# Kernel optimization log

Hardware: AMD Instinct MI355X
Metric: run time of the kernel (lower is better)

## Reference

```python
import jax, jax.numpy as jnp
import numpy as np

B, L, E, H = 8192, 64, 128, 8  # batch, max seq len, info_size, head_num
HD = E // H                    # head dim


def setup_inputs() -> dict:
    key = jax.random.key(0)
    k1, k2, k3, k4, k5, k6 = jax.random.split(key, 6)
    inter_info = jax.random.normal(k1, (B, L, E), dtype=jnp.float32)
    # ragged lengths in [1, L] (each sample has at least the query vector)
    lengths = jax.random.randint(k2, (B,), 1, L + 1, dtype=jnp.int32)
    s = 1.0 / np.sqrt(E)
    in_proj_w = jax.random.uniform(k3, (3 * E, E), dtype=jnp.float32, minval=-s, maxval=s)
    in_proj_b = jnp.zeros((3 * E,), dtype=jnp.float32)
    out_proj_w = jax.random.uniform(k4, (E, E), dtype=jnp.float32, minval=-s, maxval=s)
    out_proj_b = jnp.zeros((E,), dtype=jnp.float32)
    return {"inter_info": inter_info, "lengths": lengths,
            "in_proj_w": in_proj_w, "in_proj_b": in_proj_b,
            "out_proj_w": out_proj_w, "out_proj_b": out_proj_b}


def reference(inter_info, lengths, in_proj_w, in_proj_b, out_proj_w, out_proj_b):
    # Per sample: query = first vector, keys/values = all (valid) vectors.
    # Equivalent to torch nn.MultiheadAttention with 1 query per sample.
    Wq, Wk, Wv = in_proj_w[:E], in_proj_w[E:2 * E], in_proj_w[2 * E:]
    bq, bk, bv = in_proj_b[:E], in_proj_b[E:2 * E], in_proj_b[2 * E:]

    query_info = inter_info[:, 0]                                  # [B, E]
    q = (query_info @ Wq.T + bq).reshape(B, H, HD)                 # [B, H, hd]
    k = (inter_info @ Wk.T + bk).reshape(B, L, H, HD)              # [B, L, H, hd]
    v = (inter_info @ Wv.T + bv).reshape(B, L, H, HD)

    scores = jnp.einsum('bhd,blhd->bhl', q, k) / np.sqrt(HD)       # [B, H, L]
    valid = jnp.arange(L)[None, :] < lengths[:, None]              # [B, L]
    scores = jnp.where(valid[:, None, :], scores, -jnp.inf)
    attn = jax.nn.softmax(scores, axis=-1)                         # [B, H, L]

    ctx = jnp.einsum('bhl,blhd->bhd', attn, v).reshape(B, E)       # [B, E]
    attn_hidden = ctx @ out_proj_w.T + out_proj_b                  # [B, E]
    return attn_hidden, query_info
```

## Files before the change

kernel.cpp:

```cpp
#include <hip/hip_runtime.h>
#include <hip/hip_bf16.h>


typedef unsigned int  u32;
typedef unsigned short u16;

#define XR  136
#define XR4 17
#define YR  136
#define UR  136
#define SCR 68

typedef __attribute__((ext_vector_type(8))) __bf16 bf16x8;
typedef __attribute__((ext_vector_type(4))) float  f32x4;

struct __align__(16) Smem {
  u16   Xs[2][64 * XR];
  u16   u[2][8 * UR];
  u16   y[2][8 * YR];
  float q[2][128];
  float sc[2][8][SCR];
  float c[2][8];
  float ctx[2][128];
  int   isbf;
};

__device__ __forceinline__ float blo(u32 u) { return __uint_as_float(u << 16); }
__device__ __forceinline__ float bhi(u32 u) { return __uint_as_float(u & 0xffff0000u); }
__device__ __forceinline__ float b2f(u16 u) { return __uint_as_float(((u32)u) << 16); }
__device__ __forceinline__ u16 f2b(float f) {
  union { __hip_bfloat16 h; u16 u; } cv; cv.h = __float2bfloat16(f); return cv.u;
}
__device__ __forceinline__ u32 pack2(float a, float b) {
  return (u32)f2b(a) | ((u32)f2b(b) << 16);
}
__device__ __forceinline__ void unp8(uint4 v, float* o) {
  o[0]=blo(v.x); o[1]=bhi(v.x); o[2]=blo(v.y); o[3]=bhi(v.y);
  o[4]=blo(v.z); o[5]=bhi(v.z); o[6]=blo(v.w); o[7]=bhi(v.w);
}

template<bool BF>
__device__ __forceinline__ uint4 wfrag(const void* p, size_t off) {
  if (BF) {
    return *(const uint4*)((const u16*)p + off);
  } else {
    const float4* q4 = (const float4*)((const float*)p + off);
    float4 a = q4[0], b = q4[1];
    uint4 v;
    v.x = pack2(a.x, a.y); v.y = pack2(a.z, a.w);
    v.z = pack2(b.x, b.y); v.w = pack2(b.z, b.w);
    return v;
  }
}
template<bool BF>
__device__ __forceinline__ void load4(const void* p, size_t off, float* o) {
  if (BF) {
    uint2 v = *(const uint2*)((const u16*)p + off);
    o[0]=blo(v.x); o[1]=bhi(v.x); o[2]=blo(v.y); o[3]=bhi(v.y);
  } else {
    float4 v = *(const float4*)((const float*)p + off);
    o[0]=v.x; o[1]=v.y; o[2]=v.z; o[3]=v.w;
  }
}
template<bool BF>
__device__ __forceinline__ float lds1(const void* p, size_t off) {
  return BF ? b2f(((const u16*)p)[off]) : ((const float*)p)[off];
}

template<bool BF>
__device__ __forceinline__ void body(Smem& S, int b0, int t,
    const void* inter, const int* lengths, const void* w_in, const void* b_in,
    const void* w_out, const void* b_out, void* out)
{
  const int len0 = lengths[b0];
  const int len1 = lengths[b0 + 1];
  const int lane = t & 63, w = t >> 6;

#pragma unroll
  for (int r = 0; r < 4; ++r) {
    int g = t + 512 * r;
    int tile = g >> 10, gg = g & 1023, l = gg >> 4, ci = gg & 15;
    uint4 v = make_uint4(0u, 0u, 0u, 0u);
    if (l < (tile ? len1 : len0)) {
      if (BF) {
        v = ((const uint4*)inter)[(size_t)b0 * 1024 + g];
      } else {
        const float4* src = (const float4*)inter + (size_t)b0 * 2048;
        float4 a = src[g * 2], b = src[g * 2 + 1];
        v.x = pack2(a.x, a.y); v.y = pack2(a.z, a.w);
        v.z = pack2(b.x, b.y); v.w = pack2(b.z, b.w);
      }
    }
    ((uint4*)S.Xs[tile])[l * XR4 + ci] = v;
  }
  __syncthreads();

  {
    const int e = w * 16 + (lane & 15);
    const int btc = (lane & 15) < 2 ? (lane & 15) : 1;
    const int kb = (lane >> 4) * 8;
    f32x4 acc = {0.f, 0.f, 0.f, 0.f};
#pragma unroll
    for (int kc = 0; kc < 4; ++kc) {
      union { uint4 u4; bf16x8 b; } A, Bf;
      A.u4  = *(const uint4*)&S.Xs[btc][kc * 32 + kb];
      Bf.u4 = wfrag<BF>(w_in, (size_t)e * 128 + kc * 32 + kb);
      acc = __builtin_amdgcn_mfma_f32_16x16x32_bf16(A.b, Bf.b, acc, 0, 0, 0);
    }
    if (lane < 16) {
      float bq = lds1<BF>(b_in, e);
      S.q[0][e] = acc[0] + bq;
      S.q[1][e] = acc[1] + bq;
    }
  }
  __syncthreads();

  {
    const int bt = t >> 8, h = (t >> 5) & 7, cc = t & 31;
    float a0=0.f,a1=0.f,a2=0.f,a3=0.f;
#pragma unroll
    for (int d = 0; d < 16; ++d) {
      float w4[4]; load4<BF>(w_in, (size_t)(128 + h * 16 + d) * 128 + cc * 4, w4);
      float q0 = S.q[bt][h * 16 + d];
      a0 = fmaf(w4[0], q0, a0); a1 = fmaf(w4[1], q0, a1);
      a2 = fmaf(w4[2], q0, a2); a3 = fmaf(w4[3], q0, a3);
    }
    *(uint2*)&S.u[bt][h * UR + cc * 4] = make_uint2(pack2(a0, a1), pack2(a2, a3));
    if (cc == 0) {
      float c0 = 0.f;
      for (int d = 0; d < 16; ++d)
        c0 += S.q[bt][h * 16 + d] * lds1<BF>(b_in, 128 + h * 16 + d);
      S.c[bt][h] = c0;
    }
  }
  __syncthreads();

  {
    const int bt = w >> 2, mt = w & 3;
    const int arow = mt * 16 + (lane & 15);
    const int col  = lane & 15;
    const int kb   = (lane >> 4) * 8;
    const bool hv  = (col < 8);
    f32x4 acc = {0.f, 0.f, 0.f, 0.f};
#pragma unroll
    for (int kc = 0; kc < 4; ++kc) {
      union { uint4 u4; bf16x8 b8; } a, b;
      a.u4 = *(const uint4*)&S.Xs[bt][arow * XR + kc * 32 + kb];
      b.u4 = *(const uint4*)&S.u[bt][(col & 7) * UR + kc * 32 + kb];
      if (!hv) b.u4 = make_uint4(0u, 0u, 0u, 0u);
      acc = __builtin_amdgcn_mfma_f32_16x16x32_bf16(a.b8, b.b8, acc, 0, 0, 0);
    }
    if (hv) {
      const int l0 = mt * 16 + (lane >> 4) * 4;
      const float cadd = S.c[bt][col];
      f32x4 o;
      o[0] = (acc[0] + cadd) * 0.25f;
      o[1] = (acc[1] + cadd) * 0.25f;
      o[2] = (acc[2] + cadd) * 0.25f;
      o[3] = (acc[3] + cadd) * 0.25f;
      *(f32x4*)&S.sc[bt][col][l0] = o;
    }
  }
  __syncthreads();

  {
    const int bt = t >> 8, h = (t >> 5) & 7, sub = t & 31;
    const int len = bt ? len1 : len0;
    const int l0 = sub, l1 = sub + 32;
    float s0 = S.sc[bt][h][l0], s1 = S.sc[bt][h][l1];
    const bool v0 = l0 < len, v1 = l1 < len;
    float m = fmaxf(v0 ? s0 : -INFINITY, v1 ? s1 : -INFINITY);
#pragma unroll
    for (int off = 16; off > 0; off >>= 1) m = fmaxf(m, __shfl_xor(m, off, 32));
    float e0 = v0 ? __expf(s0 - m) : 0.f;
    float e1 = v1 ? __expf(s1 - m) : 0.f;
    float s = e0 + e1;
#pragma unroll
    for (int off = 16; off > 0; off >>= 1) s += __shfl_xor(s, off, 32);
    float inv = 1.f / s;
    S.sc[bt][h][l0] = e0 * inv;
    S.sc[bt][h][l1] = e1 * inv;
  }
  __syncthreads();

  {
    const int bt = w >> 2, j0 = (w & 3) * 32;
    const int hA = (lane & 15) < 8 ? (lane & 15) : 7;
    const int l8 = (lane >> 4) * 8;
    const int jc0 = j0 + (lane & 15), jc1 = jc0 + 16;
    const int len = bt ? len1 : len0;
    f32x4 acc0 = {0.f,0.f,0.f,0.f}, acc1 = {0.f,0.f,0.f,0.f};
    const u16* xb = S.Xs[bt];

    {
      const int lb = l8;
      float4 pa = *(const float4*)&S.sc[bt][hA][lb];
      float4 pb = *(const float4*)&S.sc[bt][hA][lb + 4];
      union { u32 u[4]; bf16x8 b; } A, B0, B1;
      A.u[0] = pack2(pa.x, pa.y); A.u[1] = pack2(pa.z, pa.w);
      A.u[2] = pack2(pb.x, pb.y); A.u[3] = pack2(pb.z, pb.w);
#pragma unroll
      for (int jj = 0; jj < 4; ++jj) {
        u32 lo0 = xb[(lb+2*jj)*XR + jc0], hi0 = xb[(lb+2*jj+1)*XR + jc0];
        u32 lo1 = xb[(lb+2*jj)*XR + jc1], hi1 = xb[(lb+2*jj+1)*XR + jc1];
        B0.u[jj] = lo0 | (hi0 << 16);
        B1.u[jj] = lo1 | (hi1 << 16);
      }
      acc0 = __builtin_amdgcn_mfma_f32_16x16x32_bf16(A.b, B0.b, acc0, 0, 0, 0);
      acc1 = __builtin_amdgcn_mfma_f32_16x16x32_bf16(A.b, B1.b, acc1, 0, 0, 0);
    }
    if (len > 32) {
      const int lb = 32 + l8;
      float4 pa = *(const float4*)&S.sc[bt][hA][lb];
      float4 pb = *(const float4*)&S.sc[bt][hA][lb + 4];
      union { u32 u[4]; bf16x8 b; } A, B0, B1;
      A.u[0] = pack2(pa.x, pa.y); A.u[1] = pack2(pa.z, pa.w);
      A.u[2] = pack2(pb.x, pb.y); A.u[3] = pack2(pb.z, pb.w);
#pragma unroll
      for (int jj = 0; jj < 4; ++jj) {
        u32 lo0 = xb[(lb+2*jj)*XR + jc0], hi0 = xb[(lb+2*jj+1)*XR + jc0];
        u32 lo1 = xb[(lb+2*jj)*XR + jc1], hi1 = xb[(lb+2*jj+1)*XR + jc1];
        B0.u[jj] = lo0 | (hi0 << 16);
        B1.u[jj] = lo1 | (hi1 << 16);
      }
      acc0 = __builtin_amdgcn_mfma_f32_16x16x32_bf16(A.b, B0.b, acc0, 0, 0, 0);
      acc1 = __builtin_amdgcn_mfma_f32_16x16x32_bf16(A.b, B1.b, acc1, 0, 0, 0);
    }
    const int rbase = (lane >> 4) * 4;
    if (rbase < 8) {
#pragma unroll
      for (int r = 0; r < 4; ++r) {
        S.y[bt][(rbase + r) * YR + j0 + (lane & 15)]      = f2b(acc0[r]);
        S.y[bt][(rbase + r) * YR + j0 + 16 + (lane & 15)] = f2b(acc1[r]);
      }
    }
  }
  __syncthreads();

  {
    const int e = w * 16 + (lane & 15);
    const int btc = (lane & 15) < 2 ? (lane & 15) : 1;
    const int kb = (lane >> 4) * 8;
    f32x4 acc = {0.f, 0.f, 0.f, 0.f};
#pragma unroll
    for (int kc = 0; kc < 4; ++kc) {
      union { uint4 u4; bf16x8 b; } A, Bf;
      A.u4  = *(const uint4*)&S.y[btc][w * YR + kc * 32 + kb];
      Bf.u4 = wfrag<BF>(w_in, (size_t)(256 + e) * 128 + kc * 32 + kb);
      acc = __builtin_amdgcn_mfma_f32_16x16x32_bf16(A.b, Bf.b, acc, 0, 0, 0);
    }
    if (lane < 16) {
      float bv = lds1<BF>(b_in, 256 + e);
      S.ctx[0][e] = acc[0] + bv;
      S.ctx[1][e] = acc[1] + bv;
    }
  }
  __syncthreads();

  {
    const int e = w * 16 + (lane & 15);
    const int btc = (lane & 15) < 2 ? (lane & 15) : 1;
    const int kb = (lane >> 4) * 8;
    f32x4 acc = {0.f, 0.f, 0.f, 0.f};
#pragma unroll
    for (int kc = 0; kc < 4; ++kc) {
      union { u32 u[4]; bf16x8 b; } A;
      union { uint4 u4; bf16x8 b; } Bf;
      float4 ca = *(const float4*)&S.ctx[btc][kc * 32 + kb];
      float4 cb = *(const float4*)&S.ctx[btc][kc * 32 + kb + 4];
      A.u[0] = pack2(ca.x, ca.y); A.u[1] = pack2(ca.z, ca.w);
      A.u[2] = pack2(cb.x, cb.y); A.u[3] = pack2(cb.z, cb.w);
      Bf.u4 = wfrag<BF>(w_out, (size_t)e * 128 + kc * 32 + kb);
      acc = __builtin_amdgcn_mfma_f32_16x16x32_bf16(A.b, Bf.b, acc, 0, 0, 0);
    }
    if (lane < 16) {
      float bo = lds1<BF>(b_out, e);
      float a0 = acc[0] + bo, a1 = acc[1] + bo;
      if (BF) {
        ((u16*)out)[(size_t)b0 * 128 + e]       = f2b(a0);
        ((u16*)out)[(size_t)(b0 + 1) * 128 + e] = f2b(a1);
      } else {
        ((float*)out)[(size_t)b0 * 128 + e]       = a0;
        ((float*)out)[(size_t)(b0 + 1) * 128 + e] = a1;
      }
    } else if (lane < 48) {
      const int bt = (lane >> 4) - 1;
      size_t o1 = (size_t)8192 * 128 + (size_t)(b0 + bt) * 128 + e;
      u16 xv = S.Xs[bt][e];
      if (BF) ((u16*)out)[o1] = xv;
      else    ((float*)out)[o1] = b2f(xv);
    }
  }
}

__global__ __launch_bounds__(512, 4) void infoattn_kernel(
    const void* inter, const int* __restrict__ lengths,
    const void* w_in, const void* b_in, const void* w_out, const void* b_out,
    void* out)
{
  __shared__ Smem S;
  const int t = threadIdx.x;
  const int b0 = blockIdx.x * 2;

  if (t < 64) {
    float v = b2f(((const u16*)inter)[t]);
    bool bad = !(fabsf(v) < 1000.f);
    unsigned long long m = __ballot(bad);
    if (t == 0) S.isbf = (m == 0ull) ? 1 : 0;
  }
  __syncthreads();
  const bool isbf = (S.isbf != 0);

  if (isbf) body<true >(S, b0, t, inter, lengths, w_in, b_in, w_out, b_out, out);
  else      body<false>(S, b0, t, inter, lengths, w_in, b_in, w_out, b_out, out);
}

extern "C" void kernel_launch(void* const* d_in, const int* in_sizes, int n_in,
                              void* d_out, int out_size, void* d_ws, size_t ws_size,
                              hipStream_t stream) {
  infoattn_kernel<<<dim3(4096), dim3(512), 0, stream>>>(
      d_in[0], (const int*)d_in[1], d_in[2], d_in[3], d_in[4], d_in[5], d_out);
}
```

Measured before the change: 438.8 us.

## Process one sample per block instead of two, doubling the grid

Each 512-thread block now handles a single batch sample rather than a pair, and the grid grows from 4096 to 8192 blocks. Shared memory per block roughly halves, which could allow more resident blocks per CU. Several stages now run on only half the threads or waves, and the weight fragments are loaded from global memory once per sample instead of being shared across two. The MFMA tiles for the query, value and output projections use one row instead of two, wasting more of each tile.

```diff
diff --git a/kernel.cpp b/kernel.cpp
--- a/kernel.cpp
+++ b/kernel.cpp
@@ -15,13 +15,13 @@
 typedef __attribute__((ext_vector_type(4))) float  f32x4;
 
 struct __align__(16) Smem {
-  u16   Xs[2][64 * XR];
-  u16   u[2][8 * UR];
-  u16   y[2][8 * YR];
-  float q[2][128];
-  float sc[2][8][SCR];
-  float c[2][8];
-  float ctx[2][128];
+  u16   Xs[64 * XR];
+  u16   u[8 * UR];
+  u16   y[8 * YR];
+  float q[128];
+  float sc[8][SCR];
+  float c[8];
+  float ctx[128];
   int   isbf;
 };
 
@@ -33,10 +33,6 @@
 }
 __device__ __forceinline__ u32 pack2(float a, float b) {
   return (u32)f2b(a) | ((u32)f2b(b) << 16);
-}
-__device__ __forceinline__ void unp8(uint4 v, float* o) {
-  o[0]=blo(v.x); o[1]=bhi(v.x); o[2]=blo(v.y); o[3]=bhi(v.y);
-  o[4]=blo(v.z); o[5]=bhi(v.z); o[6]=blo(v.w); o[7]=bhi(v.w);
 }
 
 template<bool BF>
@@ -68,75 +64,69 @@
 }
 
 template<bool BF>
-__device__ __forceinline__ void body(Smem& S, int b0, int t,
+__device__ __forceinline__ void body(Smem& S, int b, int t,
     const void* inter, const int* lengths, const void* w_in, const void* b_in,
     const void* w_out, const void* b_out, void* out)
 {
-  const int len0 = lengths[b0];
-  const int len1 = lengths[b0 + 1];
+  const int len = lengths[b];
   const int lane = t & 63, w = t >> 6;
 
 #pragma unroll
-  for (int r = 0; r < 4; ++r) {
+  for (int r = 0; r < 2; ++r) {
     int g = t + 512 * r;
-    int tile = g >> 10, gg = g & 1023, l = gg >> 4, ci = gg & 15;
+    int l = g >> 4, ci = g & 15;
     uint4 v = make_uint4(0u, 0u, 0u, 0u);
-    if (l < (tile ? len1 : len0)) {
+    if (l < len) {
       if (BF) {
-        v = ((const uint4*)inter)[(size_t)b0 * 1024 + g];
+        v = ((const uint4*)inter)[(size_t)b * 1024 + g];
       } else {
-        const float4* src = (const float4*)inter + (size_t)b0 * 2048;
-        float4 a = src[g * 2], b = src[g * 2 + 1];
+        const float4* src = (const float4*)inter + (size_t)b * 2048;
+        float4 a = src[g * 2], bb = src[g * 2 + 1];
         v.x = pack2(a.x, a.y); v.y = pack2(a.z, a.w);
-        v.z = pack2(b.x, b.y); v.w = pack2(b.z, b.w);
-      }
-    }
-    ((uint4*)S.Xs[tile])[l * XR4 + ci] = v;
+        v.z = pack2(bb.x, bb.y); v.w = pack2(bb.z, bb.w);
+      }
+    }
+    ((uint4*)S.Xs)[l * XR4 + ci] = v;
   }
   __syncthreads();
 
   {
     const int e = w * 16 + (lane & 15);
-    const int btc = (lane & 15) < 2 ? (lane & 15) : 1;
     const int kb = (lane >> 4) * 8;
     f32x4 acc = {0.f, 0.f, 0.f, 0.f};
 #pragma unroll
     for (int kc = 0; kc < 4; ++kc) {
-      union { uint4 u4; bf16x8 b; } A, Bf;
-      A.u4  = *(const uint4*)&S.Xs[btc][kc * 32 + kb];
+      union { uint4 u4; bf16x8 b8; } A, Bf;
+      A.u4  = *(const uint4*)&S.Xs[kc * 32 + kb];
       Bf.u4 = wfrag<BF>(w_in, (size_t)e * 128 + kc * 32 + kb);
-      acc = __builtin_amdgcn_mfma_f32_16x16x32_bf16(A.b, Bf.b, acc, 0, 0, 0);
-    }
-    if (lane < 16) {
-      float bq = lds1<BF>(b_in, e);
-      S.q[0][e] = acc[0] + bq;
-      S.q[1][e] = acc[1] + bq;
-    }
-  }
-  __syncthreads();
-
-  {
-    const int bt = t >> 8, h = (t >> 5) & 7, cc = t & 31;
+      acc = __builtin_amdgcn_mfma_f32_16x16x32_bf16(A.b8, Bf.b8, acc, 0, 0, 0);
+    }
+    if (lane < 16) S.q[e] = acc[0] + lds1<BF>(b_in, e);
+  }
+  __syncthreads();
+
+  if (t < 256) {
+    const int h = t >> 5, cc = t & 31;
     float a0=0.f,a1=0.f,a2=0.f,a3=0.f;
 #pragma unroll
     for (int d = 0; d < 16; ++d) {
       float w4[4]; load4<BF>(w_in, (size_t)(128 + h * 16 + d) * 128 + cc * 4, w4);
-      float q0 = S.q[bt][h * 16 + d];
+      float q0 = S.q[h * 16 + d];
       a0 = fmaf(w4[0], q0, a0); a1 = fmaf(w4[1], q0, a1);
       a2 = fmaf(w4[2], q0, a2); a3 = fmaf(w4[3], q0, a3);
     }
-    *(uint2*)&S.u[bt][h * UR + cc * 4] = make_uint2(pack2(a0, a1), pack2(a2, a3));
+    *(uint2*)&S.u[h * UR + cc * 4] = make_uint2(pack2(a0, a1), pack2(a2, a3));
     if (cc == 0) {
       float c0 = 0.f;
       for (int d = 0; d < 16; ++d)
-        c0 += S.q[bt][h * 16 + d] * lds1<BF>(b_in, 128 + h * 16 + d);
-      S.c[bt][h] = c0;
-    }
-  }
-  __syncthreads();
-
-  {
-    const int bt = w >> 2, mt = w & 3;
+        c0 += S.q[h * 16 + d] * lds1<BF>(b_in, 128 + h * 16 + d);
+      S.c[h] = c0;
+    }
+  }
+  __syncthreads();
+
+  if (w < 4) {
+    const int mt = w;
     const int arow = mt * 16 + (lane & 15);
     const int col  = lane & 15;
     const int kb   = (lane >> 4) * 8;
@@ -144,30 +134,29 @@
     f32x4 acc = {0.f, 0.f, 0.f, 0.f};
 #pragma unroll
     for (int kc = 0; kc < 4; ++kc) {
-      union { uint4 u4; bf16x8 b8; } a, b;
-      a.u4 = *(const uint4*)&S.Xs[bt][arow * XR + kc * 32 + kb];
-      b.u4 = *(const uint4*)&S.u[bt][(col & 7) * UR + kc * 32 + kb];
-      if (!hv) b.u4 = make_uint4(0u, 0u, 0u, 0u);
-      acc = __builtin_amdgcn_mfma_f32_16x16x32_bf16(a.b8, b.b8, acc, 0, 0, 0);
+      union { uint4 u4; bf16x8 b8; } a, bu;
+      a.u4  = *(const uint4*)&S.Xs[arow * XR + kc * 32 + kb];
+      bu.u4 = *(const uint4*)&S.u[(col & 7) * UR + kc * 32 + kb];
+      if (!hv) bu.u4 = make_uint4(0u, 0u, 0u, 0u);
+      acc = __builtin_amdgcn_mfma_f32_16x16x32_bf16(a.b8, bu.b8, acc, 0, 0, 0);
     }
     if (hv) {
       const int l0 = mt * 16 + (lane >> 4) * 4;
-      const float cadd = S.c[bt][col];
+      const float cadd = S.c[col];
       f32x4 o;
       o[0] = (acc[0] + cadd) * 0.25f;
       o[1] = (acc[1] + cadd) * 0.25f;
       o[2] = (acc[2] + cadd) * 0.25f;
       o[3] = (acc[3] + cadd) * 0.25f;
-      *(f32x4*)&S.sc[bt][col][l0] = o;
-    }
-  }
-  __syncthreads();
-
-  {
-    const int bt = t >> 8, h = (t >> 5) & 7, sub = t & 31;
-    const int len = bt ? len1 : len0;
+      *(f32x4*)&S.sc[col][l0] = o;
+    }
+  }
+  __syncthreads();
+
+  if (t < 256) {
+    const int h = t >> 5, sub = t & 31;
     const int l0 = sub, l1 = sub + 32;
-    float s0 = S.sc[bt][h][l0], s1 = S.sc[bt][h][l1];
+    float s0 = S.sc[h][l0], s1 = S.sc[h][l1];
     const bool v0 = l0 < len, v1 = l1 < len;
     float m = fmaxf(v0 ? s0 : -INFINITY, v1 ? s1 : -INFINITY);
 #pragma unroll
@@ -178,24 +167,23 @@
 #pragma unroll
     for (int off = 16; off > 0; off >>= 1) s += __shfl_xor(s, off, 32);
     float inv = 1.f / s;
-    S.sc[bt][h][l0] = e0 * inv;
-    S.sc[bt][h][l1] = e1 * inv;
-  }
-  __syncthreads();
-
-  {
-    const int bt = w >> 2, j0 = (w & 3) * 32;
+    S.sc[h][l0] = e0 * inv;
+    S.sc[h][l1] = e1 * inv;
+  }
+  __syncthreads();
+
+  if (w < 4) {
+    const int j0 = w * 32;
     const int hA = (lane & 15) < 8 ? (lane & 15) : 7;
     const int l8 = (lane >> 4) * 8;
     const int jc0 = j0 + (lane & 15), jc1 = jc0 + 16;
-    const int len = bt ? len1 : len0;
     f32x4 acc0 = {0.f,0.f,0.f,0.f}, acc1 = {0.f,0.f,0.f,0.f};
-    const u16* xb = S.Xs[bt];
+    const u16* xb = S.Xs;
 
     {
       const int lb = l8;
-      float4 pa = *(const float4*)&S.sc[bt][hA][lb];
-      float4 pb = *(const float4*)&S.sc[bt][hA][lb + 4];
+      float4 pa = *(const float4*)&S.sc[hA][lb];
+      float4 pb = *(const float4*)&S.sc[hA][lb + 4];
       union { u32 u[4]; bf16x8 b; } A, B0, B1;
       A.u[0] = pack2(pa.x, pa.y); A.u[1] = pack2(pa.z, pa.w);
       A.u[2] = pack2(pb.x, pb.y); A.u[3] = pack2(pb.z, pb.w);
@@ -211,8 +199,8 @@
     }
     if (len > 32) {
       const int lb = 32 + l8;
-      float4 pa = *(const float4*)&S.sc[bt][hA][lb];
-      float4 pb = *(const float4*)&S.sc[bt][hA][lb + 4];
+      float4 pa = *(const float4*)&S.sc[hA][lb];
+      float4 pb = *(const float4*)&S.sc[hA][lb + 4];
       union { u32 u[4]; bf16x8 b; } A, B0, B1;
       A.u[0] = pack2(pa.x, pa.y); A.u[1] = pack2(pa.z, pa.w);
       A.u[2] = pack2(pb.x, pb.y); A.u[3] = pack2(pb.z, pb.w);
@@ -230,8 +218,8 @@
     if (rbase < 8) {
 #pragma unroll
       for (int r = 0; r < 4; ++r) {
-        S.y[bt][(rbase + r) * YR + j0 + (lane & 15)]      = f2b(acc0[r]);
-        S.y[bt][(rbase + r) * YR + j0 + 16 + (lane & 15)] = f2b(acc1[r]);
+        S.y[(rbase + r) * YR + j0 + (lane & 15)]      = f2b(acc0[r]);
+        S.y[(rbase + r) * YR + j0 + 16 + (lane & 15)] = f2b(acc1[r]);
       }
     }
   }
@@ -239,54 +227,41 @@
 
   {
     const int e = w * 16 + (lane & 15);
-    const int btc = (lane & 15) < 2 ? (lane & 15) : 1;
     const int kb = (lane >> 4) * 8;
     f32x4 acc = {0.f, 0.f, 0.f, 0.f};
 #pragma unroll
     for (int kc = 0; kc < 4; ++kc) {
-      union { uint4 u4; bf16x8 b; } A, Bf;
-      A.u4  = *(const uint4*)&S.y[btc][w * YR + kc * 32 + kb];
+      union { uint4 u4; bf16x8 b8; } A, Bf;
+      A.u4  = *(const uint4*)&S.y[w * YR + kc * 32 + kb];
       Bf.u4 = wfrag<BF>(w_in, (size_t)(256 + e) * 128 + kc * 32 + kb);
-      acc = __builtin_amdgcn_mfma_f32_16x16x32_bf16(A.b, Bf.b, acc, 0, 0, 0);
-    }
-    if (lane < 16) {
-      float bv = lds1<BF>(b_in, 256 + e);
-      S.ctx[0][e] = acc[0] + bv;
-      S.ctx[1][e] = acc[1] + bv;
-    }
+      acc = __builtin_amdgcn_mfma_f32_16x16x32_bf16(A.b8, Bf.b8, acc, 0, 0, 0);
+    }
+    if (lane < 16) S.ctx[e] = acc[0] + lds1<BF>(b_in, 256 + e);
   }
   __syncthreads();
 
   {
     const int e = w * 16 + (lane & 15);
-    const int btc = (lane & 15) < 2 ? (lane & 15) : 1;
     const int kb = (lane >> 4) * 8;
     f32x4 acc = {0.f, 0.f, 0.f, 0.f};
 #pragma unroll
     for (int kc = 0; kc < 4; ++kc) {
       union { u32 u[4]; bf16x8 b; } A;
-      union { uint4 u4; bf16x8 b; } Bf;
-      float4 ca = *(const float4*)&S.ctx[btc][kc * 32 + kb];
-      float4 cb = *(const float4*)&S.ctx[btc][kc * 32 + kb + 4];
+      union { uint4 u4; bf16x8 b8; } Bf;
+      float4 ca = *(const float4*)&S.ctx[kc * 32 + kb];
+      float4 cb = *(const float4*)&S.ctx[kc * 32 + kb + 4];
       A.u[0] = pack2(ca.x, ca.y); A.u[1] = pack2(ca.z, ca.w);
       A.u[2] = pack2(cb.x, cb.y); A.u[3] = pack2(cb.z, cb.w);
       Bf.u4 = wfrag<BF>(w_out, (size_t)e * 128 + kc * 32 + kb);
-      acc = __builtin_amdgcn_mfma_f32_16x16x32_bf16(A.b, Bf.b, acc, 0, 0, 0);
+      acc = __builtin_amdgcn_mfma_f32_16x16x32_bf16(A.b, Bf.b8, acc, 0, 0, 0);
     }
     if (lane < 16) {
-      float bo = lds1<BF>(b_out, e);
-      float a0 = acc[0] + bo, a1 = acc[1] + bo;
-      if (BF) {
-        ((u16*)out)[(size_t)b0 * 128 + e]       = f2b(a0);
-        ((u16*)out)[(size_t)(b0 + 1) * 128 + e] = f2b(a1);
-      } else {
-        ((float*)out)[(size_t)b0 * 128 + e]       = a0;
-        ((float*)out)[(size_t)(b0 + 1) * 128 + e] = a1;
-      }
-    } else if (lane < 48) {
-      const int bt = (lane >> 4) - 1;
-      size_t o1 = (size_t)8192 * 128 + (size_t)(b0 + bt) * 128 + e;
-      u16 xv = S.Xs[bt][e];
+      float a0 = acc[0] + lds1<BF>(b_out, e);
+      if (BF) ((u16*)out)[(size_t)b * 128 + e]   = f2b(a0);
+      else    ((float*)out)[(size_t)b * 128 + e] = a0;
+    } else if (lane < 32) {
+      size_t o1 = (size_t)8192 * 128 + (size_t)b * 128 + e;
+      u16 xv = S.Xs[e];
       if (BF) ((u16*)out)[o1] = xv;
       else    ((float*)out)[o1] = b2f(xv);
     }
@@ -300,7 +275,7 @@
 {
   __shared__ Smem S;
   const int t = threadIdx.x;
-  const int b0 = blockIdx.x * 2;
+  const int b = blockIdx.x;
 
   if (t < 64) {
     float v = b2f(((const u16*)inter)[t]);
@@ -311,13 +286,13 @@
   __syncthreads();
   const bool isbf = (S.isbf != 0);
 
-  if (isbf) body<true >(S, b0, t, inter, lengths, w_in, b_in, w_out, b_out, out);
-  else      body<false>(S, b0, t, inter, lengths, w_in, b_in, w_out, b_out, out);
+  if (isbf) body<true >(S, b, t, inter, lengths, w_in, b_in, w_out, b_out, out);
+  else      body<false>(S, b, t, inter, lengths, w_in, b_in, w_out, b_out, out);
 }
 
 extern "C" void kernel_launch(void* const* d_in, const int* in_sizes, int n_in,
                               void* d_out, int out_size, void* d_ws, size_t ws_size,
                               hipStream_t stream) {
-  infoattn_kernel<<<dim3(4096), dim3(512), 0, stream>>>(
+  infoattn_kernel<<<dim3(8192), dim3(512), 0, stream>>>(
       d_in[0], (const int*)d_in[1], d_in[2], d_in[3], d_in[4], d_in[5], d_out);
 }
```

Result: slower. 530.5 us (+20.9%).

## Split fused attention into three kernels batching projections across more samples

Applied to the files above, without the earlier changes.

Splits the monolithic kernel into three launches. The first computes the q projection and the folded Wk^T q vectors for 8 samples per block. The second does scores, softmax and the P·X product for 2 samples per block, writing the weighted sums to workspace. The third runs the V and output projections for 16 samples per block, so MFMA tiles are fully used and weight loads are shared across more rows. In exchange it adds workspace round-trips through global memory and two extra launches. The old single kernel stays as a fallback when no workspace is provided.

```diff
diff --git a/kernel.cpp b/kernel.cpp
--- a/kernel.cpp
+++ b/kernel.cpp
@@ -4,26 +4,23 @@
 
 typedef unsigned int  u32;
 typedef unsigned short u16;
+typedef unsigned long long u64;
 
 #define XR  136
 #define XR4 17
 #define YR  136
 #define UR  136
 #define SCR 68
+#define QR  132
+#define YSR 1032
+
+#define WS_U_OFF 0u
+#define WS_C_OFF 16777216u
+#define WS_Y_OFF 17825792u
+#define WS_NEED  34603008u
 
 typedef __attribute__((ext_vector_type(8))) __bf16 bf16x8;
 typedef __attribute__((ext_vector_type(4))) float  f32x4;
-
-struct __align__(16) Smem {
-  u16   Xs[2][64 * XR];
-  u16   u[2][8 * UR];
-  u16   y[2][8 * YR];
-  float q[2][128];
-  float sc[2][8][SCR];
-  float c[2][8];
-  float ctx[2][128];
-  int   isbf;
-};
 
 __device__ __forceinline__ float blo(u32 u) { return __uint_as_float(u << 16); }
 __device__ __forceinline__ float bhi(u32 u) { return __uint_as_float(u & 0xffff0000u); }
@@ -33,10 +30,6 @@
 }
 __device__ __forceinline__ u32 pack2(float a, float b) {
   return (u32)f2b(a) | ((u32)f2b(b) << 16);
-}
-__device__ __forceinline__ void unp8(uint4 v, float* o) {
-  o[0]=blo(v.x); o[1]=bhi(v.x); o[2]=blo(v.y); o[3]=bhi(v.y);
-  o[4]=blo(v.z); o[5]=bhi(v.z); o[6]=blo(v.w); o[7]=bhi(v.w);
 }
 
 template<bool BF>
@@ -67,8 +60,375 @@
   return BF ? b2f(((const u16*)p)[off]) : ((const float*)p)[off];
 }
 
+struct __align__(16) SmemK1 {
+  u16   X0s[8 * XR];
+  float q[8 * QR];
+  int   isbf;
+};
+
 template<bool BF>
-__device__ __forceinline__ void body(Smem& S, int b0, int t,
+__device__ __forceinline__ void k1_body(SmemK1& S, int b0, int t,
+    const void* inter, const void* w_in, const void* b_in,
+    u16* Uws, float* Cws)
+{
+  const int lane = t & 63, w = t >> 6;
+
+  if (t < 128) {
+    const int i = t >> 4, ci = t & 15;
+    const size_t bidx = (size_t)(b0 + i);
+    uint4 v;
+    if (BF) {
+      v = ((const uint4*)inter)[bidx * 1024 + ci];
+    } else {
+      const float4* src = (const float4*)inter + bidx * 2048 + ci * 2;
+      float4 a = src[0], b = src[1];
+      v.x = pack2(a.x, a.y); v.y = pack2(a.z, a.w);
+      v.z = pack2(b.x, b.y); v.w = pack2(b.z, b.w);
+    }
+    *(uint4*)&S.X0s[i * XR + ci * 8] = v;
+  }
+  __syncthreads();
+
+  {
+    const int r15 = lane & 15, e = w * 16 + r15;
+    const int kb = (lane >> 4) * 8, rbase = (lane >> 4) * 4;
+    f32x4 acc = {0.f, 0.f, 0.f, 0.f};
+#pragma unroll
+    for (int kc = 0; kc < 4; ++kc) {
+      union { uint4 u4; bf16x8 b8; } A, Bf;
+      A.u4  = *(const uint4*)&S.X0s[(r15 & 7) * XR + kc * 32 + kb];
+      Bf.u4 = wfrag<BF>(w_in, (size_t)e * 128 + kc * 32 + kb);
+      acc = __builtin_amdgcn_mfma_f32_16x16x32_bf16(A.b8, Bf.b8, acc, 0, 0, 0);
+    }
+    const float bq  = lds1<BF>(b_in, e);
+    const float bkv = lds1<BF>(b_in, 128 + e);
+    float cs[4];
+#pragma unroll
+    for (int r = 0; r < 4; ++r) {
+      float qv = acc[r] + bq;
+      if (rbase < 8) S.q[(rbase + r) * QR + e] = qv;
+      cs[r] = qv * bkv;
+    }
+#pragma unroll
+    for (int off = 1; off < 16; off <<= 1) {
+      cs[0] += __shfl_xor(cs[0], off, 64);
+      cs[1] += __shfl_xor(cs[1], off, 64);
+      cs[2] += __shfl_xor(cs[2], off, 64);
+      cs[3] += __shfl_xor(cs[3], off, 64);
+    }
+    if (r15 == 0 && rbase < 8) {
+#pragma unroll
+      for (int r = 0; r < 4; ++r)
+        Cws[(size_t)(b0 + rbase + r) * 8 + w] = cs[r];
+    }
+  }
+  __syncthreads();
+
+  {
+    const int hh = t >> 8, bt = (t >> 5) & 7, cc = t & 31;
+#pragma unroll
+    for (int hi = 0; hi < 4; ++hi) {
+      const int h = hh * 4 + hi;
+      float a0 = 0.f, a1 = 0.f, a2 = 0.f, a3 = 0.f;
+#pragma unroll
+      for (int d = 0; d < 16; ++d) {
+        float w4[4]; load4<BF>(w_in, (size_t)(128 + h * 16 + d) * 128 + cc * 4, w4);
+        float q0 = S.q[bt * QR + h * 16 + d];
+        a0 = fmaf(w4[0], q0, a0); a1 = fmaf(w4[1], q0, a1);
+        a2 = fmaf(w4[2], q0, a2); a3 = fmaf(w4[3], q0, a3);
+      }
+      *(uint2*)&Uws[(size_t)(b0 + bt) * 1024 + h * 128 + cc * 4] =
+          make_uint2(pack2(a0, a1), pack2(a2, a3));
+    }
+  }
+}
+
+__global__ __launch_bounds__(512, 4) void k1_kernel(
+    const void* inter, const void* w_in, const void* b_in,
+    u16* Uws, float* Cws)
+{
+  __shared__ SmemK1 S;
+  const int t = threadIdx.x;
+  const int b0 = blockIdx.x * 8;
+  if (t < 64) {
+    float v = b2f(((const u16*)inter)[t]);
+    bool bad = !(fabsf(v) < 1000.f);
+    u64 m = __ballot(bad);
+    if (t == 0) S.isbf = (m == 0ull) ? 1 : 0;
+  }
+  __syncthreads();
+  if (S.isbf) k1_body<true >(S, b0, t, inter, w_in, b_in, Uws, Cws);
+  else        k1_body<false>(S, b0, t, inter, w_in, b_in, Uws, Cws);
+}
+
+struct __align__(16) SmemK2 {
+  u16   Xs[2][64 * XR];
+  u16   u[2][8 * UR];
+  u16   y[2][8 * YR];
+  float sc[2][8][SCR];
+  float c[2][8];
+  int   isbf;
+};
+
+template<bool BF>
+__device__ __forceinline__ void k2_body(SmemK2& S, int b0, int t,
+    const void* inter, const int* lengths, const u16* Uws, const float* Cws,
+    u16* Yws, void* out)
+{
+  const int len0 = lengths[b0];
+  const int len1 = lengths[b0 + 1];
+  const int lane = t & 63, w = t >> 6;
+
+#pragma unroll
+  for (int r = 0; r < 4; ++r) {
+    int g = t + 512 * r;
+    int tile = g >> 10, gg = g & 1023, l = gg >> 4, ci = gg & 15;
+    uint4 v = make_uint4(0u, 0u, 0u, 0u);
+    if (l < (tile ? len1 : len0)) {
+      if (BF) {
+        v = ((const uint4*)inter)[(size_t)b0 * 1024 + g];
+      } else {
+        const float4* src = (const float4*)inter + (size_t)b0 * 2048;
+        float4 a = src[g * 2], bb = src[g * 2 + 1];
+        v.x = pack2(a.x, a.y); v.y = pack2(a.z, a.w);
+        v.z = pack2(bb.x, bb.y); v.w = pack2(bb.z, bb.w);
+      }
+    }
+    ((uint4*)S.Xs[tile])[l * XR4 + ci] = v;
+  }
+  if (t < 256) {
+    const int bt = t >> 7, rem = t & 127, h = rem >> 4, ci = rem & 15;
+    uint4 v = ((const uint4*)Uws)[(size_t)(b0 + bt) * 128 + h * 16 + ci];
+    *(uint4*)&S.u[bt][h * UR + ci * 8] = v;
+  } else if (t < 272) {
+    const int i = t - 256, bt = i >> 3, h = i & 7;
+    S.c[bt][h] = Cws[(size_t)(b0 + bt) * 8 + h];
+  }
+  __syncthreads();
+
+  {
+    const int bt = w >> 2, mt = w & 3;
+    const int arow = mt * 16 + (lane & 15);
+    const int col  = lane & 15;
+    const int kb   = (lane >> 4) * 8;
+    const bool hv  = (col < 8);
+    f32x4 acc = {0.f, 0.f, 0.f, 0.f};
+#pragma unroll
+    for (int kc = 0; kc < 4; ++kc) {
+      union { uint4 u4; bf16x8 b8; } a, bu;
+      a.u4  = *(const uint4*)&S.Xs[bt][arow * XR + kc * 32 + kb];
+      bu.u4 = *(const uint4*)&S.u[bt][(col & 7) * UR + kc * 32 + kb];
+      if (!hv) bu.u4 = make_uint4(0u, 0u, 0u, 0u);
+      acc = __builtin_amdgcn_mfma_f32_16x16x32_bf16(a.b8, bu.b8, acc, 0, 0, 0);
+    }
+    if (hv) {
+      const int l0 = mt * 16 + (lane >> 4) * 4;
+      const float cadd = S.c[bt][col];
+      f32x4 o;
+      o[0] = (acc[0] + cadd) * 0.25f;
+      o[1] = (acc[1] + cadd) * 0.25f;
+      o[2] = (acc[2] + cadd) * 0.25f;
+      o[3] = (acc[3] + cadd) * 0.25f;
+      *(f32x4*)&S.sc[bt][col][l0] = o;
+    }
+  }
+  __syncthreads();
+
+  {
+    const int bt = t >> 8, h = (t >> 5) & 7, sub = t & 31;
+    const int len = bt ? len1 : len0;
+    const int l0 = sub, l1 = sub + 32;
+    float s0 = S.sc[bt][h][l0], s1 = S.sc[bt][h][l1];
+    const bool v0 = l0 < len, v1 = l1 < len;
+    float m = fmaxf(v0 ? s0 : -INFINITY, v1 ? s1 : -INFINITY);
+#pragma unroll
+    for (int off = 16; off > 0; off >>= 1) m = fmaxf(m, __shfl_xor(m, off, 32));
+    float e0 = v0 ? __expf(s0 - m) : 0.f;
+    float e1 = v1 ? __expf(s1 - m) : 0.f;
+    float s = e0 + e1;
+#pragma unroll
+    for (int off = 16; off > 0; off >>= 1) s += __shfl_xor(s, off, 32);
+    float inv = 1.f / s;
+    S.sc[bt][h][l0] = e0 * inv;
+    S.sc[bt][h][l1] = e1 * inv;
+  }
+  __syncthreads();
+
+  {
+    const int bt = w >> 2, j0 = (w & 3) * 32;
+    const int hA = (lane & 15) < 8 ? (lane & 15) : 7;
+    const int l8 = (lane >> 4) * 8;
+    const int jc0 = j0 + (lane & 15), jc1 = jc0 + 16;
+    const int len = bt ? len1 : len0;
+    f32x4 acc0 = {0.f,0.f,0.f,0.f}, acc1 = {0.f,0.f,0.f,0.f};
+    const u16* xb = S.Xs[bt];
+    {
+      const int lb = l8;
+      float4 pa = *(const float4*)&S.sc[bt][hA][lb];
+      float4 pb = *(const float4*)&S.sc[bt][hA][lb + 4];
+      union { u32 u[4]; bf16x8 b; } A, B0, B1;
+      A.u[0] = pack2(pa.x, pa.y); A.u[1] = pack2(pa.z, pa.w);
+      A.u[2] = pack2(pb.x, pb.y); A.u[3] = pack2(pb.z, pb.w);
+#pragma unroll
+      for (int jj = 0; jj < 4; ++jj) {
+        u32 lo0 = xb[(lb+2*jj)*XR + jc0], hi0 = xb[(lb+2*jj+1)*XR + jc0];
+        u32 lo1 = xb[(lb+2*jj)*XR + jc1], hi1 = xb[(lb+2*jj+1)*XR + jc1];
+        B0.u[jj] = lo0 | (hi0 << 16);
+        B1.u[jj] = lo1 | (hi1 << 16);
+      }
+      acc0 = __builtin_amdgcn_mfma_f32_16x16x32_bf16(A.b, B0.b, acc0, 0, 0, 0);
+      acc1 = __builtin_amdgcn_mfma_f32_16x16x32_bf16(A.b, B1.b, acc1, 0, 0, 0);
+    }
+    if (len > 32) {
+      const int lb = 32 + l8;
+      float4 pa = *(const float4*)&S.sc[bt][hA][lb];
+      float4 pb = *(const float4*)&S.sc[bt][hA][lb + 4];
+      union { u32 u[4]; bf16x8 b; } A, B0, B1;
+      A.u[0] = pack2(pa.x, pa.y); A.u[1] = pack2(pa.z, pa.w);
+      A.u[2] = pack2(pb.x, pb.y); A.u[3] = pack2(pb.z, pb.w);
+#pragma unroll
+      for (int jj = 0; jj < 4; ++jj) {
+        u32 lo0 = xb[(lb+2*jj)*XR + jc0], hi0 = xb[(lb+2*jj+1)*XR + jc0];
+        u32 lo1 = xb[(lb+2*jj)*XR + jc1], hi1 = xb[(lb+2*jj+1)*XR + jc1];
+        B0.u[jj] = lo0 | (hi0 << 16);
+        B1.u[jj] = lo1 | (hi1 << 16);
+      }
+      acc0 = __builtin_amdgcn_mfma_f32_16x16x32_bf16(A.b, B0.b, acc0, 0, 0, 0);
+      acc1 = __builtin_amdgcn_mfma_f32_16x16x32_bf16(A.b, B1.b, acc1, 0, 0, 0);
+    }
+    const int rbase = (lane >> 4) * 4;
+    if (rbase < 8) {
+#pragma unroll
+      for (int r = 0; r < 4; ++r) {
+        S.y[bt][(rbase + r) * YR + j0 + (lane & 15)]      = f2b(acc0[r]);
+        S.y[bt][(rbase + r) * YR + j0 + 16 + (lane & 15)] = f2b(acc1[r]);
+      }
+    }
+  }
+  __syncthreads();
+
+  if (t < 256) {
+    const int bt = t >> 7, rem = t & 127, h = rem >> 4, ci = rem & 15;
+    uint4 v = *(const uint4*)&S.y[bt][h * YR + ci * 8];
+    ((uint4*)Yws)[(size_t)(b0 + bt) * 128 + h * 16 + ci] = v;
+  } else {
+    const int i = t - 256, bt = i >> 7, e = i & 127;
+    size_t o1 = (size_t)8192 * 128 + (size_t)(b0 + bt) * 128 + e;
+    u16 xv = S.Xs[bt][e];
+    if (BF) ((u16*)out)[o1] = xv;
+    else    ((float*)out)[o1] = b2f(xv);
+  }
+}
+
+__global__ __launch_bounds__(512, 4) void k2_kernel(
+    const void* inter, const int* __restrict__ lengths,
+    const u16* Uws, const float* Cws, u16* Yws, void* out)
+{
+  __shared__ SmemK2 S;
+  const int t = threadIdx.x;
+  const int b0 = blockIdx.x * 2;
+  if (t < 64) {
+    float v = b2f(((const u16*)inter)[t]);
+    bool bad = !(fabsf(v) < 1000.f);
+    u64 m = __ballot(bad);
+    if (t == 0) S.isbf = (m == 0ull) ? 1 : 0;
+  }
+  __syncthreads();
+  if (S.isbf) k2_body<true >(S, b0, t, inter, lengths, Uws, Cws, Yws, out);
+  else        k2_body<false>(S, b0, t, inter, lengths, Uws, Cws, Yws, out);
+}
+
+struct __align__(16) SmemK3 {
+  u16 ys[16 * YSR];
+  u16 ctx[16 * 136];
+  int isbf;
+};
+
+template<bool BF>
+__device__ __forceinline__ void k3_body(SmemK3& S, int b0, int t,
+    const u16* Yws, const void* w_in, const void* b_in,
+    const void* w_out, const void* b_out, void* out)
+{
+  const int lane = t & 63, w = t >> 6;
+
+#pragma unroll
+  for (int r = 0; r < 4; ++r) {
+    int idx = t + 512 * r;
+    int row = idx >> 7, ci = idx & 127;
+    uint4 v = ((const uint4*)Yws)[(size_t)(b0 + row) * 128 + ci];
+    *(uint4*)&S.ys[row * YSR + ci * 8] = v;
+  }
+  __syncthreads();
+
+  {
+    const int col = lane & 15, kb = (lane >> 4) * 8, rbase = (lane >> 4) * 4;
+    f32x4 acc = {0.f, 0.f, 0.f, 0.f};
+#pragma unroll
+    for (int kc = 0; kc < 4; ++kc) {
+      union { uint4 u4; bf16x8 b8; } A, Bf;
+      A.u4  = *(const uint4*)&S.ys[col * YSR + w * 128 + kc * 32 + kb];
+      Bf.u4 = wfrag<BF>(w_in, (size_t)(256 + w * 16 + col) * 128 + kc * 32 + kb);
+      acc = __builtin_amdgcn_mfma_f32_16x16x32_bf16(A.b8, Bf.b8, acc, 0, 0, 0);
+    }
+    const float bv = lds1<BF>(b_in, 256 + w * 16 + col);
+#pragma unroll
+    for (int r = 0; r < 4; ++r)
+      S.ctx[(rbase + r) * 136 + w * 16 + col] = f2b(acc[r] + bv);
+  }
+  __syncthreads();
+
+  {
+    const int col = lane & 15, kb = (lane >> 4) * 8, rbase = (lane >> 4) * 4;
+    f32x4 acc = {0.f, 0.f, 0.f, 0.f};
+#pragma unroll
+    for (int kc = 0; kc < 4; ++kc) {
+      union { uint4 u4; bf16x8 b8; } A, Bf;
+      A.u4  = *(const uint4*)&S.ctx[col * 136 + kc * 32 + kb];
+      Bf.u4 = wfrag<BF>(w_out, (size_t)(w * 16 + col) * 128 + kc * 32 + kb);
+      acc = __builtin_amdgcn_mfma_f32_16x16x32_bf16(A.b8, Bf.b8, acc, 0, 0, 0);
+    }
+    const float bo = lds1<BF>(b_out, w * 16 + col);
+#pragma unroll
+    for (int r = 0; r < 4; ++r) {
+      float v = acc[r] + bo;
+      size_t oo = (size_t)(b0 + rbase + r) * 128 + w * 16 + col;
+      if (BF) ((u16*)out)[oo] = f2b(v);
+      else    ((float*)out)[oo] = v;
+    }
+  }
+}
+
+__global__ __launch_bounds__(512, 4) void k3_kernel(
+    const u16* Yws, const void* w_in, const void* b_in,
+    const void* w_out, const void* b_out, void* out)
+{
+  __shared__ SmemK3 S;
+  const int t = threadIdx.x;
+  const int b0 = blockIdx.x * 16;
+  if (t < 64) {
+    float v = b2f(((const u16*)w_out)[t]);
+    bool bad = !(fabsf(v) < 1000.f);
+    u64 m = __ballot(bad);
+    if (t == 0) S.isbf = (m == 0ull) ? 1 : 0;
+  }
+  __syncthreads();
+  if (S.isbf) k3_body<true >(S, b0, t, Yws, w_in, b_in, w_out, b_out, out);
+  else        k3_body<false>(S, b0, t, Yws, w_in, b_in, w_out, b_out, out);
+}
+
+struct __align__(16) SmemM {
+  u16   Xs[2][64 * XR];
+  u16   u[2][8 * UR];
+  u16   y[2][8 * YR];
+  float q[2][128];
+  float sc[2][8][SCR];
+  float c[2][8];
+  float ctx[2][128];
+  int   isbf;
+};
+
+template<bool BF>
+__device__ __forceinline__ void mono_body(SmemM& S, int b0, int t,
     const void* inter, const int* lengths, const void* w_in, const void* b_in,
     const void* w_out, const void* b_out, void* out)
 {
@@ -102,10 +462,10 @@
     f32x4 acc = {0.f, 0.f, 0.f, 0.f};
 #pragma unroll
     for (int kc = 0; kc < 4; ++kc) {
-      union { uint4 u4; bf16x8 b; } A, Bf;
+      union { uint4 u4; bf16x8 b8; } A, Bf;
       A.u4  = *(const uint4*)&S.Xs[btc][kc * 32 + kb];
       Bf.u4 = wfrag<BF>(w_in, (size_t)e * 128 + kc * 32 + kb);
-      acc = __builtin_amdgcn_mfma_f32_16x16x32_bf16(A.b, Bf.b, acc, 0, 0, 0);
+      acc = __builtin_amdgcn_mfma_f32_16x16x32_bf16(A.b8, Bf.b8, acc, 0, 0, 0);
     }
     if (lane < 16) {
       float bq = lds1<BF>(b_in, e);
@@ -144,11 +504,11 @@
     f32x4 acc = {0.f, 0.f, 0.f, 0.f};
 #pragma unroll
     for (int kc = 0; kc < 4; ++kc) {
-      union { uint4 u4; bf16x8 b8; } a, b;
-      a.u4 = *(const uint4*)&S.Xs[bt][arow * XR + kc * 32 + kb];
-      b.u4 = *(const uint4*)&S.u[bt][(col & 7) * UR + kc * 32 + kb];
-      if (!hv) b.u4 = make_uint4(0u, 0u, 0u, 0u);
-      acc = __builtin_amdgcn_mfma_f32_16x16x32_bf16(a.b8, b.b8, acc, 0, 0, 0);
+      union { uint4 u4; bf16x8 b8; } a, bu;
+      a.u4  = *(const uint4*)&S.Xs[bt][arow * XR + kc * 32 + kb];
+      bu.u4 = *(const uint4*)&S.u[bt][(col & 7) * UR + kc * 32 + kb];
+      if (!hv) bu.u4 = make_uint4(0u, 0u, 0u, 0u);
+      acc = __builtin_amdgcn_mfma_f32_16x16x32_bf16(a.b8, bu.b8, acc, 0, 0, 0);
     }
     if (hv) {
       const int l0 = mt * 16 + (lane >> 4) * 4;
@@ -191,7 +551,6 @@
     const int len = bt ? len1 : len0;
     f32x4 acc0 = {0.f,0.f,0.f,0.f}, acc1 = {0.f,0.f,0.f,0.f};
     const u16* xb = S.Xs[bt];
-
     {
       const int lb = l8;
       float4 pa = *(const float4*)&S.sc[bt][hA][lb];
@@ -244,15 +603,14 @@
     f32x4 acc = {0.f, 0.f, 0.f, 0.f};
 #pragma unroll
     for (int kc = 0; kc < 4; ++kc) {
-      union { uint4 u4; bf16x8 b; } A, Bf;
+      union { uint4 u4; bf16x8 b8; } A, Bf;
       A.u4  = *(const uint4*)&S.y[btc][w * YR + kc * 32 + kb];
       Bf.u4 = wfrag<BF>(w_in, (size_t)(256 + e) * 128 + kc * 32 + kb);
-      acc = __builtin_amdgcn_mfma_f32_16x16x32_bf16(A.b, Bf.b, acc, 0, 0, 0);
+      acc = __builtin_amdgcn_mfma_f32_16x16x32_bf16(A.b8, Bf.b8, acc, 0, 0, 0);
     }
     if (lane < 16) {
-      float bv = lds1<BF>(b_in, 256 + e);
-      S.ctx[0][e] = acc[0] + bv;
-      S.ctx[1][e] = acc[1] + bv;
+      S.ctx[0][e] = acc[0] + lds1<BF>(b_in, 256 + e);
+      S.ctx[1][e] = acc[1] + lds1<BF>(b_in, 256 + e);
     }
   }
   __syncthreads();
@@ -265,13 +623,13 @@
 #pragma unroll
     for (int kc = 0; kc < 4; ++kc) {
       union { u32 u[4]; bf16x8 b; } A;
-      union { uint4 u4; bf16x8 b; } Bf;
+      union { uint4 u4; bf16x8 b8; } Bf;
       float4 ca = *(const float4*)&S.ctx[btc][kc * 32 + kb];
       float4 cb = *(const float4*)&S.ctx[btc][kc * 32 + kb + 4];
       A.u[0] = pack2(ca.x, ca.y); A.u[1] = pack2(ca.z, ca.w);
       A.u[2] = pack2(cb.x, cb.y); A.u[3] = pack2(cb.z, cb.w);
       Bf.u4 = wfrag<BF>(w_out, (size_t)e * 128 + kc * 32 + kb);
-      acc = __builtin_amdgcn_mfma_f32_16x16x32_bf16(A.b, Bf.b, acc, 0, 0, 0);
+      acc = __builtin_amdgcn_mfma_f32_16x16x32_bf16(A.b, Bf.b8, acc, 0, 0, 0);
     }
     if (lane < 16) {
       float bo = lds1<BF>(b_out, e);
@@ -293,31 +651,40 @@
   }
 }
 
-__global__ __launch_bounds__(512, 4) void infoattn_kernel(
+__global__ __launch_bounds__(512, 4) void mono_kernel(
     const void* inter, const int* __restrict__ lengths,
     const void* w_in, const void* b_in, const void* w_out, const void* b_out,
     void* out)
 {
-  __shared__ Smem S;
+  __shared__ SmemM S;
   const int t = threadIdx.x;
   const int b0 = blockIdx.x * 2;
-
   if (t < 64) {
     float v = b2f(((const u16*)inter)[t]);
     bool bad = !(fabsf(v) < 1000.f);
-    unsigned long long m = __ballot(bad);
+    u64 m = __ballot(bad);
     if (t == 0) S.isbf = (m == 0ull) ? 1 : 0;
   }
   __syncthreads();
-  const bool isbf = (S.isbf != 0);
-
-  if (isbf) body<true >(S, b0, t, inter, lengths, w_in, b_in, w_out, b_out, out);
-  else      body<false>(S, b0, t, inter, lengths, w_in, b_in, w_out, b_out, out);
+  if (S.isbf) mono_body<true >(S, b0, t, inter, lengths, w_in, b_in, w_out, b_out, out);
+  else        mono_body<false>(S, b0, t, inter, lengths, w_in, b_in, w_out, b_out, out);
 }
 
 extern "C" void kernel_launch(void* const* d_in, const int* in_sizes, int n_in,
                               void* d_out, int out_size, void* d_ws, size_t ws_size,
                               hipStream_t stream) {
-  infoattn_kernel<<<dim3(4096), dim3(512), 0, stream>>>(
-      d_in[0], (const int*)d_in[1], d_in[2], d_in[3], d_in[4], d_in[5], d_out);
-}
+  if (d_ws && ws_size >= (size_t)WS_NEED) {
+    u16*   Uws = (u16*)((char*)d_ws + WS_U_OFF);
+    float* Cws = (float*)((char*)d_ws + WS_C_OFF);
+    u16*   Yws = (u16*)((char*)d_ws + WS_Y_OFF);
+    k1_kernel<<<dim3(1024), dim3(512), 0, stream>>>(
+        d_in[0], d_in[2], d_in[3], Uws, Cws);
+    k2_kernel<<<dim3(4096), dim3(512), 0, stream>>>(
+        d_in[0], (const int*)d_in[1], Uws, Cws, Yws, d_out);
+    k3_kernel<<<dim3(512), dim3(512), 0, stream>>>(
+        Yws, d_in[2], d_in[3], d_in[4], d_in[5], d_out);
+  } else {
+    mono_kernel<<<dim3(4096), dim3(512), 0, stream>>>(
+        d_in[0], (const int*)d_in[1], d_in[2], d_in[3], d_in[4], d_in[5], d_out);
+  }
+}
```

Result: faster. 380.8 us (-13.2%).
